# Performance work log

Measured on AMD Instinct MI355X. Metric: run time of the kernel, lower is better.

## Reference

```python
import jax, jax.numpy as jnp
import numpy as np

B, L, D = 4, 1024, 1024
H = 16
HD = D // H
SCALE = HD ** -0.5
LOCAL_WINDOW = 32
HALF = LOCAL_WINDOW // 2
TEMP = 1.0
PATTERN_TEMP = 1.0
THRESHOLD = 0.1
SPARSITY_RATIO = 0.3
# k for learned sparse topk (eval mode, static given L)
EFF = min(SPARSITY_RATIO, 1.0 - 10.0 / L)
K_TOP = max(1, min(L, int(L * (1.0 - EFF))))


def setup_inputs() -> dict:
    key = jax.random.key(0)
    ks = jax.random.split(key, 16)
    def xavier(k, shape, gain=1.0):
        fan_in, fan_out = shape[1], shape[0]
        a = gain * np.sqrt(6.0 / (fan_in + fan_out))
        return jax.random.uniform(k, shape, jnp.float32, -a, a)
    return {
        'x': jax.random.normal(ks[0], (B, L, D), jnp.float32),
        'w_qkv': xavier(ks[1], (3 * D, D), gain=1.0 / np.sqrt(2.0)),
        'w_proj': xavier(ks[2], (D, D)),
        'b_proj': jnp.zeros((D,), jnp.float32),
        'ps_w1': xavier(ks[3], (D, D), gain=0.5),
        'ps_b1': jnp.zeros((D,), jnp.float32),
        'ln_g': jnp.ones((D,), jnp.float32),
        'ln_b': jnp.zeros((D,), jnp.float32),
        'ps_w2': xavier(ks[4], (D // 2, D), gain=0.5),
        'ps_b2': jnp.zeros((D // 2,), jnp.float32),
        'ps_w3': xavier(ks[5], (3, D // 2), gain=0.5),
        'ps_b3': jnp.zeros((3,), jnp.float32),
        'pattern_bias': jnp.array([0.05, 0.0, -0.05], jnp.float32),
        'sparse_w': jax.random.normal(ks[6], (H, 1, 1), jnp.float32) * 0.1 + 1.0,
        'sparse_b': jnp.zeros((H, 1, 1), jnp.float32),
    }


def _forward(x, w_qkv, w_proj, b_proj, ps_w1, ps_b1, ln_g, ln_b,
             ps_w2, ps_b2, ps_w3, ps_b3, pattern_bias, sparse_w, sparse_b):
    qkv = (x @ w_qkv.T).reshape(B, L, 3, H, HD)
    qkv = jnp.transpose(qkv, (2, 0, 3, 1, 4))  # [3,B,H,L,HD]
    q, k, v = qkv[0], qkv[1], qkv[2]
    scores = jnp.einsum('bhid,bhjd->bhij', q, k) * SCALE  # [B,H,L,L]

    # pattern selector on pooled features
    pooled = (jnp.mean(x, axis=1) + jnp.max(x, axis=1)) / 2.0  # [B,D]
    h = pooled @ ps_w1.T + ps_b1
    mu = jnp.mean(h, axis=-1, keepdims=True)
    var = jnp.mean((h - mu) ** 2, axis=-1, keepdims=True)
    h = (h - mu) / jnp.sqrt(var + 1e-5) * ln_g + ln_b
    h = jax.nn.gelu(h, approximate=False)
    h = jax.nn.gelu(h @ ps_w2.T + ps_b2, approximate=False)
    logits = h @ ps_w3.T + ps_b3 + pattern_bias  # [B,3]
    pw = jax.nn.softmax(logits / PATTERN_TEMP, axis=-1)  # [B,3]

    # learned sparse mask via per-head affine + topk scatter
    s2 = scores * jnp.abs(sparse_w)[None] + sparse_b[None]  # [B,H,L,L]
    _, topk_idx = jax.lax.top_k(s2, K_TOP)  # [B,H,L,K]
    bi = jnp.arange(B)[:, None, None, None]
    hi = jnp.arange(H)[None, :, None, None]
    li = jnp.arange(L)[None, None, :, None]
    sparse_mask = jnp.zeros_like(scores).at[bi, hi, li, topk_idx].set(1.0)

    # local sliding-window mask |i-j| <= HALF
    i = jnp.arange(L)
    local = (jnp.abs(i[:, None] - i[None, :]) <= HALF).astype(jnp.float32)  # [L,L]

    combined = (pw[:, 0, None, None, None] * local[None, None]
                + pw[:, 1, None, None, None]
                + pw[:, 2, None, None, None] * sparse_mask)
    binary = combined > THRESHOLD
    scores = jnp.where(binary, scores, -jnp.inf)

    # fallback: rows fully masked attend only to themselves (score 0)
    all_masked = ~jnp.any(binary, axis=-1)  # [B,H,L]
    eye = jnp.eye(L, dtype=bool)
    scores = jnp.where(all_masked[..., None] & eye[None, None], 0.0, scores)

    attn = jax.nn.softmax(scores / TEMP, axis=-1)
    out = jnp.einsum('bhij,bhjd->bhid', attn, v)  # [B,H,L,HD]
    out = jnp.transpose(out, (0, 2, 1, 3)).reshape(B, L, D)
    return out @ w_proj.T + b_proj


def reference(x, w_qkv, w_proj, b_proj, ps_w1, ps_b1, ln_g, ln_b,
              ps_w2, ps_b2, ps_w3, ps_b3, pattern_bias, sparse_w, sparse_b):
    return _forward(x, w_qkv, w_proj, b_proj, ps_w1, ps_b1, ln_g, ln_b,
                    ps_w2, ps_b2, ps_w3, ps_b3, pattern_bias, sparse_w, sparse_b)
```

## Files before the change

### kernel.cpp

```cpp
#include <hip/hip_runtime.h>
#include <math.h>

#define KTOP_ 716
#define SCALE_ 0.125f
#define QSCALE_ 0.1803368801111731f
#define LN2_ 0.6931471805599453f

typedef float f4v __attribute__((ext_vector_type(4)));
typedef short s8v __attribute__((ext_vector_type(8)));
typedef __bf16 bf8v __attribute__((ext_vector_type(8)));

static __device__ inline unsigned short f2bf(float f) {
  unsigned u = __float_as_uint(f);
  u += 0x7fffu + ((u >> 16) & 1u);
  return (unsigned short)(u >> 16);
}
static __device__ inline unsigned short f2bfn(float f) {
  union { __bf16 b; unsigned short u; } cv;
  cv.b = (__bf16)f;
  return cv.u;
}
static __device__ inline float bf2f(unsigned short h) {
  return __uint_as_float((unsigned)h << 16);
}
static __device__ inline f4v mfma16(s8v a, s8v b, f4v c) {
  union { s8v s; bf8v b; } ua, ub;
  ua.s = a; ub.s = b;
  return __builtin_amdgcn_mfma_f32_16x16x32_bf16(ua.b, ub.b, c, 0, 0, 0);
}
static __device__ inline void gload16(const unsigned short* g, unsigned short* lbase) {
  __builtin_amdgcn_global_load_lds(
      (const __attribute__((address_space(1))) unsigned int*)g,
      (__attribute__((address_space(3))) unsigned int*)lbase, 16, 0, 0);
}

__global__ __launch_bounds__(256) void pool1(const float* __restrict__ x,
                                             float* __restrict__ psum,
                                             float* __restrict__ pmax,
                                             unsigned short* __restrict__ xs) {
  int bid = blockIdx.x;
  int b = bid >> 6, sl = bid & 63;
  int t = threadIdx.x;
  float s[4] = {0.f, 0.f, 0.f, 0.f};
  float m[4] = {-INFINITY, -INFINITY, -INFINITY, -INFINITY};
  const float* xb = x + ((size_t)b << 20) + (size_t)sl * 16 * 1024;
  unsigned short* xo = xs + ((size_t)(b * 1024 + sl * 16)) * 1024;
  for (int l = 0; l < 16; ++l) {
    #pragma unroll
    for (int dg = 0; dg < 4; ++dg) {
      float v = xb[l * 1024 + dg * 256 + t];
      s[dg] += v;
      m[dg] = fmaxf(m[dg], v);
      xo[(size_t)l * 1024 + dg * 256 + t] = f2bfn(v);
    }
  }
  #pragma unroll
  for (int dg = 0; dg < 4; ++dg) {
    psum[(size_t)bid * 1024 + dg * 256 + t] = s[dg];
    pmax[(size_t)bid * 1024 + dg * 256 + t] = m[dg];
  }
}

__global__ __launch_bounds__(256) void ps_gemv1(const float* __restrict__ psum,
                                                const float* __restrict__ pmax,
                                                const float* __restrict__ w1,
                                                const float* __restrict__ b1,
                                                float* __restrict__ h1) {
  __shared__ float pool_s[1024];
  int bid = blockIdx.x;
  int b = bid >> 4, og = bid & 15;
  int t = threadIdx.x;
  #pragma unroll
  for (int i = 0; i < 4; ++i) {
    int d = t + 256 * i;
    float s = 0.f, m = -INFINITY;
    #pragma unroll 8
    for (int sl = 0; sl < 64; ++sl) {
      s += psum[((size_t)b * 64 + sl) * 1024 + d];
      m = fmaxf(m, pmax[((size_t)b * 64 + sl) * 1024 + d]);
    }
    pool_s[d] = (s * (1.0f / 1024.0f) + m) * 0.5f;
  }
  __syncthreads();
  int ol = t >> 2, ks = t & 3;
  int o = og * 64 + ol;
  const float4* wr = (const float4*)(w1 + (size_t)o * 1024 + ks * 256);
  const float4* pp = (const float4*)(&pool_s[ks * 256]);
  float acc = 0.f;
  #pragma unroll 8
  for (int j = 0; j < 64; ++j) {
    float4 a = wr[j], p = pp[j];
    acc += a.x * p.x + a.y * p.y + a.z * p.z + a.w * p.w;
  }
  acc += __shfl_xor(acc, 1, 64);
  acc += __shfl_xor(acc, 2, 64);
  if (ks == 0) h1[b * 1024 + o] = acc + b1[o];
}

__global__ __launch_bounds__(256) void ps_gemv2(const float* __restrict__ h1,
                                                const float* __restrict__ lng,
                                                const float* __restrict__ lnb,
                                                const float* __restrict__ w2,
                                                const float* __restrict__ b2,
                                                float* __restrict__ h2) {
  __shared__ float hs[1024];
  __shared__ float red[256];
  int bid = blockIdx.x;
  int b = bid >> 3, og = bid & 7;
  int t = threadIdx.x;
  const float* hb = h1 + b * 1024;
  float v0[4];
  float ls = 0.f;
  #pragma unroll
  for (int i = 0; i < 4; ++i) { v0[i] = hb[t + 256 * i]; ls += v0[i]; }
  red[t] = ls; __syncthreads();
  for (int s = 128; s > 0; s >>= 1) { if (t < s) red[t] += red[t + s]; __syncthreads(); }
  float mean = red[0] * (1.0f / 1024.0f);
  __syncthreads();
  float lq = 0.f;
  #pragma unroll
  for (int i = 0; i < 4; ++i) { float dv = v0[i] - mean; lq += dv * dv; }
  red[t] = lq; __syncthreads();
  for (int s = 128; s > 0; s >>= 1) { if (t < s) red[t] += red[t + s]; __syncthreads(); }
  float rstd = 1.0f / sqrtf(red[0] * (1.0f / 1024.0f) + 1e-5f);
  #pragma unroll
  for (int i = 0; i < 4; ++i) {
    float v = (v0[i] - mean) * rstd * lng[t + 256 * i] + lnb[t + 256 * i];
    hs[t + 256 * i] = 0.5f * v * (1.0f + erff(v * 0.70710678118654752f));
  }
  __syncthreads();
  int ol = t >> 2, ks = t & 3;
  int o = og * 64 + ol;
  const float4* wr = (const float4*)(w2 + (size_t)o * 1024 + ks * 256);
  const float4* pp = (const float4*)(&hs[ks * 256]);
  float acc = 0.f;
  #pragma unroll 8
  for (int j = 0; j < 64; ++j) {
    float4 a = wr[j], p = pp[j];
    acc += a.x * p.x + a.y * p.y + a.z * p.z + a.w * p.w;
  }
  acc += __shfl_xor(acc, 1, 64);
  acc += __shfl_xor(acc, 2, 64);
  if (ks == 0) {
    float v = acc + b2[o];
    h2[b * 512 + o] = 0.5f * v * (1.0f + erff(v * 0.70710678118654752f));
  }
}

__global__ __launch_bounds__(256) void ps_logits(const float* __restrict__ h2,
                                                 const float* __restrict__ w3,
                                                 const float* __restrict__ b3,
                                                 const float* __restrict__ pb,
                                                 int* __restrict__ meta) {
  __shared__ float red[256];
  int b = blockIdx.x, t = threadIdx.x;
  float lgv[3];
  for (int c = 0; c < 3; ++c) {
    float p = 0.f;
    for (int i = t; i < 512; i += 256) p += h2[b * 512 + i] * w3[c * 512 + i];
    red[t] = p; __syncthreads();
    for (int s = 128; s > 0; s >>= 1) { if (t < s) red[t] += red[t + s]; __syncthreads(); }
    lgv[c] = red[0] + b3[c] + pb[c];
    __syncthreads();
  }
  if (t == 0) {
    float mx = fmaxf(lgv[0], fmaxf(lgv[1], lgv[2]));
    float e0 = __expf(lgv[0] - mx), e1 = __expf(lgv[1] - mx), e2 = __expf(lgv[2] - mx);
    float inv = 1.0f / (e0 + e1 + e2);
    float p0 = e0 * inv, p1 = e1 * inv, p2 = e2 * inv;
    float c00 = p1;
    float c10 = p0 + p1;
    float c01 = p1 + p2;
    float c11 = (p0 + p1) + p2;
    int t00 = c00 > 0.1f, t10 = c10 > 0.1f, t01 = c01 > 0.1f, t11 = c11 > 0.1f;
    meta[b * 8 + 0] = t00;
    meta[b * 8 + 1] = t10;
    meta[b * 8 + 2] = t01;
    meta[b * 8 + 3] = t11;
    meta[b * 8 + 4] = (t00 != t01) || (t10 != t11);
  }
}

__global__ __launch_bounds__(256) void prep_w(const float* __restrict__ w_qkv,
                                              const float* __restrict__ w_proj,
                                              unsigned short* __restrict__ wqs,
                                              unsigned short* __restrict__ wps) {
  int i = blockIdx.x * 256 + threadIdx.x;
  const float* src;
  unsigned short* dst;
  int idx;
  if (i < 786432) { src = w_qkv; dst = wqs; idx = i; }
  else            { src = w_proj; dst = wps; idx = i - 786432; }
  float4 v = ((const float4*)src)[idx];
  ushort4 o;
  o.x = f2bfn(v.x); o.y = f2bfn(v.y); o.z = f2bfn(v.z); o.w = f2bfn(v.w);
  *(ushort4*)(dst + (size_t)idx * 4) = o;
}

template <int MODE, int TM>
__global__ __launch_bounds__(256) void gemm_sp(
    const unsigned short* __restrict__ A, const unsigned short* __restrict__ B,
    const float* __restrict__ bias,
    unsigned short* __restrict__ qxo, unsigned short* __restrict__ kxo,
    unsigned short* __restrict__ vxo,
    float* __restrict__ out, int Nb) {
  constexpr int MFR = TM / 32;
  __shared__ unsigned short Asm[2][TM * 64];
  __shared__ unsigned short Bsm[2][128 * 64];

  int bid = blockIdx.x;
  int bm, bn;
  if (MODE == 0) {
    int xcd = bid & 7, idx = bid >> 3;
    int rb = (xcd >> 1) * 8, cb = (xcd & 1) * 12;
    int r, c;
    if (idx < 64) { r = idx & 7; c = idx >> 3; }
    else          { int j = idx - 64; r = j & 7; c = 8 + (j >> 3); }
    bm = rb + r; bn = cb + c;
  } else {
    int cpx = gridDim.x >> 3;
    int g = (bid & 7) * cpx + (bid >> 3);
    bm = g / Nb; bn = g % Nb;
  }
  size_t row0 = (size_t)bm * TM, col0 = (size_t)bn * 128;

  int tid = threadIdx.x, lane = tid & 63, wv = tid >> 6;
  int wm = (wv >> 1) * (MFR * 16), wn = (wv & 1) << 6;
  int rowg = lane >> 4, colc = lane & 15;

  f4v acc[MFR][4];
  #pragma unroll
  for (int mf = 0; mf < MFR; ++mf)
    #pragma unroll
    for (int nf = 0; nf < 4; ++nf) acc[mf][nf] = (f4v){0.f, 0.f, 0.f, 0.f};

  const unsigned short* Abase = A + row0 * 1024;
  const unsigned short* Bbase = B + col0 * 1024;

  auto STAGE = [&](int kb, int buf) {
    #pragma unroll
    for (int p = 0; p < TM / 32; ++p) {
      int idx = p * 256 + tid;
      int row = idx >> 3;
      int sc = (idx & 7) ^ (row & 7);
      gload16(Abase + (size_t)row * 1024 + kb + sc * 8,
              &Asm[buf][(size_t)(p * 256 + wv * 64) * 8]);
    }
    #pragma unroll
    for (int p = 0; p < 4; ++p) {
      int idx = p * 256 + tid;
      int row = idx >> 3;
      int sc = (idx & 7) ^ (row & 7);
      gload16(Bbase + (size_t)row * 1024 + kb + sc * 8,
              &Bsm[buf][(size_t)(p * 256 + wv * 64) * 8]);
    }
  };

  STAGE(0, 0);
  __syncthreads();
  int cur = 0;

  for (int kb = 0; kb < 1024; kb += 64) {
    if (kb + 64 < 1024) STAGE(kb + 64, cur ^ 1);
    #pragma unroll
    for (int ks = 0; ks < 2; ++ks) {
      s8v af[MFR], bf_[4];
      #pragma unroll
      for (int mf = 0; mf < MFR; ++mf) {
        int row = wm + mf * 16 + colc;
        int kby = (ks * 64 + rowg * 16) ^ ((row & 7) << 4);
        af[mf] = *(const s8v*)((const char*)&Asm[cur][0] + row * 128 + kby);
      }
      #pragma unroll
      for (int nf = 0; nf < 4; ++nf) {
        int row = wn + nf * 16 + colc;
        int kby = (ks * 64 + rowg * 16) ^ ((row & 7) << 4);
        bf_[nf] = *(const s8v*)((const char*)&Bsm[cur][0] + row * 128 + kby);
      }
      #pragma unroll
      for (int mf = 0; mf < MFR; ++mf)
        #pragma unroll
        for (int nf = 0; nf < 4; ++nf)
          acc[mf][nf] = mfma16(af[mf], bf_[nf], acc[mf][nf]);
    }
    __syncthreads();
    cur ^= 1;
  }

  if (MODE == 0) {
    int c = (int)(col0 >> 10);
    #pragma unroll
    for (int mf = 0; mf < MFR; ++mf) {
      int m0 = (int)row0 + wm + mf * 16 + rowg * 4;
      int bb = m0 >> 10, l0 = m0 & 1023;
      #pragma unroll
      for (int nf = 0; nf < 4; ++nf) {
        int n = (int)col0 + wn + nf * 16 + colc;
        int hh = (n >> 6) & 15, hd = n & 63;
        int bhl = bb * 16 + hh;
        if (c == 2) {
          ushort4 h4;
          h4.x = f2bfn(acc[mf][nf][0]);
          h4.y = f2bfn(acc[mf][nf][1]);
          h4.z = f2bfn(acc[mf][nf][2]);
          h4.w = f2bfn(acc[mf][nf][3]);
          *(ushort4*)(vxo + ((size_t)bhl * 64 + hd) * 1024 + l0) = h4;
        } else {
          unsigned short* dst = ((c == 0) ? qxo : kxo) +
                                ((size_t)bhl * 1024 + l0) * 64 + hd;
          float sc_ = (c == 0) ? QSCALE_ : 1.0f;
          #pragma unroll
          for (int r = 0; r < 4; ++r)
            dst[(size_t)r * 64] = f2bfn(acc[mf][nf][r] * sc_);
        }
      }
    }
  } else {
    #pragma unroll
    for (int mf = 0; mf < MFR; ++mf) {
      #pragma unroll
      for (int r = 0; r < 4; ++r) {
        int m = (int)row0 + wm + mf * 16 + rowg * 4 + r;
        #pragma unroll
        for (int nf = 0; nf < 4; ++nf) {
          int n = (int)col0 + wn + nf * 16 + colc;
          out[(size_t)m * 1024 + n] = acc[mf][nf][r] + bias[n];
        }
      }
    }
  }
}

__global__ __launch_bounds__(512) void attn_flash(
    const unsigned short* __restrict__ qx, const unsigned short* __restrict__ kx,
    const unsigned short* __restrict__ vx, const int* __restrict__ meta,
    unsigned short* __restrict__ ao) {
  int n = blockIdx.x;
  int bh = ((n & 7) << 3) | (n >> 6);
  int qt2 = (n >> 3) & 7;
  int b = bh >> 4, h = bh & 15;
  const int* mb = meta + b * 8;
  if (mb[4]) return;
  int t00 = mb[0], t10 = mb[1];

  int tid = threadIdx.x, lane = tid & 63, wv = tid >> 6;
  int g = lane >> 4, colc = lane & 15;
  int bq0 = qt2 * 128;
  int q0 = bq0 + wv * 16;

  if (!t10) {
    #pragma unroll
    for (int it = 0; it < 4; ++it) {
      int idx = tid + it * 512;
      int r = idx >> 4, dc = (idx & 15) * 4;
      ushort4 o;
      unsigned short* op = (unsigned short*)&o;
      #pragma unroll
      for (int j = 0; j < 4; ++j)
        op[j] = vx[((size_t)bh * 64 + dc + j) * 1024 + bq0 + r];
      *(ushort4*)(ao + ((size_t)b * 1024 + bq0 + r) * 1024 + h * 64 + dc) = o;
    }
    return;
  }
  bool local_only = !t00;

  __shared__ __align__(16) unsigned short KsmA[64 * 64];
  __shared__ __align__(16) unsigned short KsmB[64 * 64];
  __shared__ __align__(16) unsigned short VsmA[64 * 64];
  __shared__ __align__(16) unsigned short VsmB[64 * 64];
  __shared__ __align__(16) unsigned short px[8][16][64];

  const unsigned short* qb = qx + ((size_t)bh * 1024 + q0 + colc) * 64 + g * 8;
  s8v Q0 = *(const s8v*)(qb);
  s8v Q1 = *(const s8v*)(qb + 32);

  f4v O[4];
  #pragma unroll
  for (int df = 0; df < 4; ++df) O[df] = (f4v){0.f, 0.f, 0.f, 0.f};
  float m = -1e30f, lsum = 0.f;

  const unsigned short* kxb = kx + ((size_t)bh << 10) * 64;
  const unsigned short* vxb = vx + ((size_t)bh << 16);

  int jb_lo = 0, jb_hi = 15;
  if (local_only) {
    int lo = (bq0 - 16) >> 6, hi = (bq0 + 143) >> 6;
    jb_lo = lo < 0 ? 0 : lo;
    jb_hi = hi > 15 ? 15 : hi;
  }

  int srow = tid >> 3;
  int ssc = (tid & 7) ^ (srow & 7);
  auto STAGE = [&](int jb2, unsigned short* Kd, unsigned short* Vd) {
    int jc = jb2 << 6;
    unsigned short* lbase_k = Kd + (size_t)(wv * 64) * 8;
    unsigned short* lbase_v = Vd + (size_t)(wv * 64) * 8;
    gload16(kxb + (size_t)(jc + srow) * 64 + ssc * 8, lbase_k);
    gload16(vxb + (size_t)srow * 1024 + jc + ssc * 8, lbase_v);
  };

  int swk = (colc & 7) << 4;
  int sx = (colc & 7) << 1;

  auto COMPUTE = [&](int jc0, const char* Kb, const char* Vb) {
    if (local_only && (jc0 + 63 < q0 - 16 || jc0 > q0 + 31)) return;
    f4v s[4];
    __builtin_amdgcn_s_setprio(1);
    #pragma unroll
    for (int jf = 0; jf < 4; ++jf) {
      const char* kp = Kb + (jf * 16 + colc) * 128;
      s8v K0 = *(const s8v*)(kp + ((g * 16) ^ swk));
      s8v K1 = *(const s8v*)(kp + ((64 + g * 16) ^ swk));
      f4v acc = (f4v){0.f, 0.f, 0.f, 0.f};
      acc = mfma16(K0, Q0, acc);
      acc = mfma16(K1, Q1, acc);
      s[jf] = acc;
    }
    __builtin_amdgcn_s_setprio(0);

    if (local_only) {
      int i = q0 + colc;
      #pragma unroll
      for (int jf = 0; jf < 4; ++jf)
        #pragma unroll
        for (int r = 0; r < 4; ++r) {
          int j = jc0 + jf * 16 + 4 * g + r;
          int dj = i - j;
          if (dj > 16 || dj < -16) s[jf][r] = -1e30f;
        }
    }

    float cm = fmaxf(
        fmaxf(fmaxf(fmaxf(s[0][0], s[0][1]), fmaxf(s[0][2], s[0][3])),
              fmaxf(fmaxf(s[1][0], s[1][1]), fmaxf(s[1][2], s[1][3]))),
        fmaxf(fmaxf(fmaxf(s[2][0], s[2][1]), fmaxf(s[2][2], s[2][3])),
              fmaxf(fmaxf(s[3][0], s[3][1]), fmaxf(s[3][2], s[3][3]))));
    cm = fmaxf(cm, __shfl_xor(cm, 16, 64));
    cm = fmaxf(cm, __shfl_xor(cm, 32, 64));

    if (__any(cm > m + 8.0f)) {
      float mn = fmaxf(m, cm);
      float fac = __builtin_amdgcn_exp2f(m - mn);
      m = mn;
      lsum *= fac;
      float fo[4];
      #pragma unroll
      for (int r = 0; r < 4; ++r)
        fo[r] = __shfl(fac, (lane & 48) + g * 4 + r, 64);
      #pragma unroll
      for (int df = 0; df < 4; ++df)
        #pragma unroll
        for (int r = 0; r < 4; ++r) O[df][r] *= fo[r];
    }

    float psum = 0.f;
    #pragma unroll
    for (int jf = 0; jf < 4; ++jf) {
      float p0 = __builtin_amdgcn_exp2f(s[jf][0] - m);
      float p1 = __builtin_amdgcn_exp2f(s[jf][1] - m);
      float p2 = __builtin_amdgcn_exp2f(s[jf][2] - m);
      float p3 = __builtin_amdgcn_exp2f(s[jf][3] - m);
      psum += (p0 + p1) + (p2 + p3);
      ushort4 pk;
      pk.x = f2bfn(p0); pk.y = f2bfn(p1); pk.z = f2bfn(p2); pk.w = f2bfn(p3);
      *(ushort4*)&px[wv][colc][4 * ((jf * 4 + g) ^ sx)] = pk;
    }
    psum += __shfl_xor(psum, 16, 64);
    psum += __shfl_xor(psum, 32, 64);
    lsum += psum;

    s8v Pf[2];
    #pragma unroll
    for (int ks = 0; ks < 2; ++ks)
      Pf[ks] = *(const s8v*)&px[wv][colc][4 * ((ks * 8 + 2 * g) ^ sx)];
    __builtin_amdgcn_s_setprio(1);
    #pragma unroll
    for (int df = 0; df < 4; ++df) {
      const char* vp = Vb + (df * 16 + colc) * 128;
      #pragma unroll
      for (int ks = 0; ks < 2; ++ks) {
        s8v Vf = *(const s8v*)(vp + ((ks * 64 + g * 16) ^ swk));
        O[df] = mfma16(Pf[ks], Vf, O[df]);
      }
    }
    __builtin_amdgcn_s_setprio(0);
  };

  STAGE(jb_lo, KsmA, VsmA);
  __syncthreads();
  int jb = jb_lo;
  while (true) {
    if (jb + 1 <= jb_hi) STAGE(jb + 1, KsmB, VsmB);
    COMPUTE(jb << 6, (const char*)KsmA, (const char*)VsmA);
    __syncthreads();
    ++jb;
    if (jb > jb_hi) break;
    if (jb + 1 <= jb_hi) STAGE(jb + 1, KsmA, VsmA);
    COMPUTE(jb << 6, (const char*)KsmB, (const char*)VsmB);
    __syncthreads();
    ++jb;
    if (jb > jb_hi) break;
  }

  float linv[4];
  #pragma unroll
  for (int r = 0; r < 4; ++r)
    linv[r] = 1.0f / __shfl(lsum, (lane & 48) + g * 4 + r, 64);
  #pragma unroll
  for (int df = 0; df < 4; ++df) {
    #pragma unroll
    for (int r = 0; r < 4; ++r) {
      int i = q0 + g * 4 + r;
      ao[((size_t)b * 1024 + i) * 1024 + h * 64 + df * 16 + colc] =
          f2bfn(O[df][r] * linv[r]);
    }
  }
}

__global__ __launch_bounds__(256) void attn_sparse(
    const unsigned short* __restrict__ qx, const unsigned short* __restrict__ kx,
    const unsigned short* __restrict__ vx, const int* __restrict__ meta,
    unsigned short* __restrict__ ao) {
  __shared__ float S[32][1028];
  __shared__ float qs[32][68];
  __shared__ float kc[64][68];
  __shared__ float rowsum_s[32];

  int tid = threadIdx.x;
  int lane = tid & 63;
  int wv = tid >> 6;
  int id = blockIdx.x;
  int rt = id & 31;
  int h = (id >> 5) & 15;
  int b = id >> 9;
  int bh = b * 16 + h;
  int row0 = rt * 32;

  const int* mb = meta + b * 8;
  int t00 = mb[0], t10 = mb[1], t01 = mb[2], t11 = mb[3], needs = mb[4];
  if (!needs) return;

  #pragma unroll
  for (int i = 0; i < 8; ++i) {
    int idx = tid + 256 * i;
    int r = idx >> 6, d = idx & 63;
    qs[r][d] = bf2f(qx[((size_t)bh * 1024 + row0 + r) * 64 + d]);
  }

  int lr = lane >> 4, lc = lane & 15;
  int r_a = wv * 8 + lr * 2;
  int r_b = r_a + 1;

  for (int cb = 0; cb < 16; ++cb) {
    __syncthreads();
    #pragma unroll
    for (int i = 0; i < 2; ++i) {
      int idx = tid + 256 * i;
      int cc = idx >> 3, d0 = (idx & 7) * 8;
      union { s8v v; unsigned short u[8]; } kv8;
      kv8.v = *(const s8v*)(kx + ((size_t)bh * 1024 + cb * 64 + cc) * 64 + d0);
      #pragma unroll
      for (int j = 0; j < 8; ++j) kc[cc][d0 + j] = bf2f(kv8.u[j]);
    }
    __syncthreads();

    float acc0[4] = {0.f, 0.f, 0.f, 0.f};
    float acc1[4] = {0.f, 0.f, 0.f, 0.f};
    for (int dq = 0; dq < 64; dq += 4) {
      float4 qa = *(const float4*)&qs[r_a][dq];
      float4 qb = *(const float4*)&qs[r_b][dq];
      #pragma unroll
      for (int cj = 0; cj < 4; ++cj) {
        float4 kv = *(const float4*)&kc[lc + 16 * cj][dq];
        acc0[cj] += qa.x * kv.x + qa.y * kv.y + qa.z * kv.z + qa.w * kv.w;
        acc1[cj] += qb.x * kv.x + qb.y * kv.y + qb.z * kv.z + qb.w * kv.w;
      }
    }
    #pragma unroll
    for (int cj = 0; cj < 4; ++cj) {
      S[r_a][cb * 64 + lc + 16 * cj] = acc0[cj] * LN2_;
      S[r_b][cb * 64 + lc + 16 * cj] = acc1[cj] * LN2_;
    }
  }

  for (int rr = 0; rr < 8; ++rr) {
    int r = wv * 8 + rr;
    int grow = row0 + r;
    float sv[16];
    unsigned kv[16];
    #pragma unroll
    for (int i2 = 0; i2 < 16; ++i2) {
      float s = S[r][lane + 64 * i2];
      sv[i2] = s;
      unsigned u = __float_as_uint(s);
      kv[i2] = (u & 0x80000000u) ? ~u : (u | 0x80000000u);
    }
    unsigned T = 0u;
    for (int bit = 31; bit >= 0; --bit) {
      unsigned cand = T | (1u << bit);
      int cnt = 0;
      #pragma unroll
      for (int i2 = 0; i2 < 16; ++i2) cnt += (kv[i2] >= cand) ? 1 : 0;
      for (int off = 32; off; off >>= 1) cnt += __shfl_xor(cnt, off, 64);
      if (cnt >= KTOP_) T = cand;
    }
    float mx = -INFINITY;
    int kept = 0;
    unsigned kmask = 0;
    #pragma unroll
    for (int i2 = 0; i2 < 16; ++i2) {
      int j = lane + 64 * i2;
      int sp = (kv[i2] >= T) ? 1 : 0;
      int dj = grow - j;
      int lo = (dj <= 16 && dj >= -16) ? 1 : 0;
      int keep = sp ? (lo ? t11 : t01) : (lo ? t10 : t00);
      kept += keep;
      if (keep) { kmask |= (1u << i2); mx = fmaxf(mx, sv[i2]); }
    }
    for (int off = 32; off; off >>= 1) {
      mx = fmaxf(mx, __shfl_xor(mx, off, 64));
      kept += __shfl_xor(kept, off, 64);
    }
    if (kept == 0) {
      #pragma unroll
      for (int i2 = 0; i2 < 16; ++i2) {
        int j = lane + 64 * i2;
        S[r][j] = (j == grow) ? 1.0f : 0.0f;
      }
      if (lane == 0) rowsum_s[r] = 1.0f;
    } else {
      float sum = 0.f;
      #pragma unroll
      for (int i2 = 0; i2 < 16; ++i2) {
        float p = ((kmask >> i2) & 1u) ? __expf(sv[i2] - mx) : 0.0f;
        sum += p;
        S[r][lane + 64 * i2] = p;
      }
      for (int off = 32; off; off >>= 1) sum += __shfl_xor(sum, off, 64);
      if (lane == 0) rowsum_s[r] = sum;
    }
  }

  int ld = lane & 15;
  int d0 = ld * 4;
  float4 oa0 = make_float4(0.f, 0.f, 0.f, 0.f);
  float4 oa1 = make_float4(0.f, 0.f, 0.f, 0.f);
  for (int vb = 0; vb < 16; ++vb) {
    __syncthreads();
    #pragma unroll
    for (int i = 0; i < 2; ++i) {
      int idx = tid + 256 * i;
      int d = idx >> 3, c0 = (idx & 7) * 8;
      union { s8v v; unsigned short u[8]; } vv8;
      vv8.v = *(const s8v*)(vx + ((size_t)bh * 64 + d) * 1024 + vb * 64 + c0);
      #pragma unroll
      for (int j = 0; j < 8; ++j) kc[c0 + j][d] = bf2f(vv8.u[j]);
    }
    __syncthreads();
    for (int cq = 0; cq < 64; cq += 4) {
      float4 pa = *(const float4*)&S[r_a][vb * 64 + cq];
      float4 pb = *(const float4*)&S[r_b][vb * 64 + cq];
      float par[4] = {pa.x, pa.y, pa.z, pa.w};
      float pbr[4] = {pb.x, pb.y, pb.z, pb.w};
      #pragma unroll
      for (int tt = 0; tt < 4; ++tt) {
        float4 vv = *(const float4*)&kc[cq + tt][d0];
        oa0.x += par[tt] * vv.x; oa0.y += par[tt] * vv.y;
        oa0.z += par[tt] * vv.z; oa0.w += par[tt] * vv.w;
        oa1.x += pbr[tt] * vv.x; oa1.y += pbr[tt] * vv.y;
        oa1.z += pbr[tt] * vv.z; oa1.w += pbr[tt] * vv.w;
      }
    }
  }
  float inv0 = 1.0f / rowsum_s[r_a];
  float inv1 = 1.0f / rowsum_s[r_b];
  ushort4 o0, o1;
  unsigned short* o0p = (unsigned short*)&o0;
  unsigned short* o1p = (unsigned short*)&o1;
  float v0[4] = {oa0.x * inv0, oa0.y * inv0, oa0.z * inv0, oa0.w * inv0};
  float v1[4] = {oa1.x * inv1, oa1.y * inv1, oa1.z * inv1, oa1.w * inv1};
  #pragma unroll
  for (int j = 0; j < 4; ++j) {
    o0p[j] = f2bf(v0[j]);
    o1p[j] = f2bf(v1[j]);
  }
  *(ushort4*)(ao + ((size_t)b * 1024 + row0 + r_a) * 1024 + h * 64 + d0) = o0;
  *(ushort4*)(ao + ((size_t)b * 1024 + row0 + r_b) * 1024 + h * 64 + d0) = o1;
}

__global__ __launch_bounds__(256) void pool_kernel(const float* __restrict__ x,
                                                   float* __restrict__ pooled) {
  int g = blockIdx.x * 256 + threadIdx.x;
  int b = g >> 10, d = g & 1023;
  const float* xp = x + ((size_t)b << 20) + d;
  float s = 0.f, m = -INFINITY;
  #pragma unroll 4
  for (int l = 0; l < 1024; ++l) {
    float v = xp[(size_t)l << 10];
    s += v;
    m = fmaxf(m, v);
  }
  pooled[g] = (s * (1.0f / 1024.0f) + m) * 0.5f;
}

__global__ __launch_bounds__(256) void qkv_gemm(const float* __restrict__ X,
                                                const float* __restrict__ W,
                                                float* __restrict__ qw,
                                                float* __restrict__ kw,
                                                float* __restrict__ vw) {
  __shared__ float As[8][128];
  __shared__ float Bs[8][128];
  int tid = threadIdx.x;
  int row0 = blockIdx.y * 128, col0 = blockIdx.x * 128;
  int lr = tid >> 1;
  int lk = (tid & 1) * 4;
  int ty = tid >> 4, tx = tid & 15;
  float acc[8][8] = {};

  for (int kb = 0; kb < 1024; kb += 8) {
    float4 a4 = *(const float4*)(X + (size_t)(row0 + lr) * 1024 + kb + lk);
    float4 b4 = *(const float4*)(W + (size_t)(col0 + lr) * 1024 + kb + lk);
    __syncthreads();
    As[lk + 0][lr] = a4.x; As[lk + 1][lr] = a4.y; As[lk + 2][lr] = a4.z; As[lk + 3][lr] = a4.w;
    Bs[lk + 0][lr] = b4.x; Bs[lk + 1][lr] = b4.y; Bs[lk + 2][lr] = b4.z; Bs[lk + 3][lr] = b4.w;
    __syncthreads();
    #pragma unroll
    for (int kk = 0; kk < 8; ++kk) {
      float av[8], bv[8];
      #pragma unroll
      for (int i = 0; i < 8; ++i) av[i] = As[kk][ty * 8 + i];
      #pragma unroll
      for (int j = 0; j < 8; ++j) bv[j] = Bs[kk][tx * 8 + j];
      #pragma unroll
      for (int i = 0; i < 8; ++i)
        #pragma unroll
        for (int j = 0; j < 8; ++j) acc[i][j] += av[i] * bv[j];
    }
  }
  #pragma unroll
  for (int i = 0; i < 8; ++i) {
    int m = row0 + ty * 8 + i;
    int bb = m >> 10, l = m & 1023;
    #pragma unroll
    for (int j = 0; j < 8; j += 4) {
      int n = col0 + tx * 8 + j;
      int c = n >> 10;
      int hh = (n >> 6) & 15;
      int hd = n & 63;
      float* base = (c == 0) ? qw : (c == 1) ? kw : vw;
      float* dst = base + ((size_t)(bb * 16 + hh) * 1024 + l) * 64 + hd;
      *(float4*)dst = make_float4(acc[i][j], acc[i][j + 1], acc[i][j + 2], acc[i][j + 3]);
    }
  }
}

__global__ __launch_bounds__(256) void proj_gemm(const float* __restrict__ A,
                                                 const float* __restrict__ W,
                                                 const float* __restrict__ bias,
                                                 float* __restrict__ out) {
  __shared__ float As[8][128];
  __shared__ float Bs[8][128];
  int tid = threadIdx.x;
  int row0 = blockIdx.y * 128, col0 = blockIdx.x * 128;
  int lr = tid >> 1;
  int lk = (tid & 1) * 4;
  int ty = tid >> 4, tx = tid & 15;
  float acc[8][8] = {};

  for (int kb = 0; kb < 1024; kb += 8) {
    float4 a4 = *(const float4*)(A + (size_t)(row0 + lr) * 1024 + kb + lk);
    float4 b4 = *(const float4*)(W + (size_t)(col0 + lr) * 1024 + kb + lk);
    __syncthreads();
    As[lk + 0][lr] = a4.x; As[lk + 1][lr] = a4.y; As[lk + 2][lr] = a4.z; As[lk + 3][lr] = a4.w;
    Bs[lk + 0][lr] = b4.x; Bs[lk + 1][lr] = b4.y; Bs[lk + 2][lr] = b4.z; Bs[lk + 3][lr] = b4.w;
    __syncthreads();
    #pragma unroll
    for (int kk = 0; kk < 8; ++kk) {
      float av[8], bv[8];
      #pragma unroll
      for (int i = 0; i < 8; ++i) av[i] = As[kk][ty * 8 + i];
      #pragma unroll
      for (int j = 0; j < 8; ++j) bv[j] = Bs[kk][tx * 8 + j];
      #pragma unroll
      for (int i = 0; i < 8; ++i)
        #pragma unroll
        for (int j = 0; j < 8; ++j) acc[i][j] += av[i] * bv[j];
    }
  }
  #pragma unroll
  for (int i = 0; i < 8; ++i) {
    int m = row0 + ty * 8 + i;
    #pragma unroll
    for (int j = 0; j < 8; j += 4) {
      int n = col0 + tx * 8 + j;
      *(float4*)(out + (size_t)m * 1024 + n) =
          make_float4(acc[i][j] + bias[n], acc[i][j + 1] + bias[n + 1],
                      acc[i][j + 2] + bias[n + 2], acc[i][j + 3] + bias[n + 3]);
    }
  }
}

__global__ __launch_bounds__(256) void pattern_kernel(
    const float* __restrict__ pooled,
    const float* __restrict__ w1, const float* __restrict__ b1,
    const float* __restrict__ lng, const float* __restrict__ lnb,
    const float* __restrict__ w2, const float* __restrict__ b2,
    const float* __restrict__ w3, const float* __restrict__ b3,
    const float* __restrict__ pb, int* __restrict__ meta) {
  __shared__ float pool_s[1024];
  __shared__ float h1[1024];
  __shared__ float h2[512];
  __shared__ float red[256];
  int b = blockIdx.x, t = threadIdx.x;

  for (int i = t; i < 1024; i += 256) pool_s[i] = pooled[b * 1024 + i];
  __syncthreads();
  for (int o = t; o < 1024; o += 256) {
    float acc = b1[o];
    const float* wr = w1 + (size_t)o * 1024;
    for (int k = 0; k < 1024; ++k) acc += pool_s[k] * wr[k];
    h1[o] = acc;
  }
  __syncthreads();
  float ls = 0.f;
  for (int i = t; i < 1024; i += 256) ls += h1[i];
  red[t] = ls; __syncthreads();
  for (int s = 128; s > 0; s >>= 1) { if (t < s) red[t] += red[t + s]; __syncthreads(); }
  float mean = red[0] * (1.0f / 1024.0f);
  __syncthreads();
  float lq = 0.f;
  for (int i = t; i < 1024; i += 256) { float dv = h1[i] - mean; lq += dv * dv; }
  red[t] = lq; __syncthreads();
  for (int s = 128; s > 0; s >>= 1) { if (t < s) red[t] += red[t + s]; __syncthreads(); }
  float var = red[0] * (1.0f / 1024.0f);
  float rstd = 1.0f / sqrtf(var + 1e-5f);
  __syncthreads();
  for (int i = t; i < 1024; i += 256) {
    float v = (h1[i] - mean) * rstd * lng[i] + lnb[i];
    h1[i] = 0.5f * v * (1.0f + erff(v * 0.70710678118654752f));
  }
  __syncthreads();
  for (int o = t; o < 512; o += 256) {
    float acc = b2[o];
    const float* wr = w2 + (size_t)o * 1024;
    for (int k = 0; k < 1024; ++k) acc += h1[k] * wr[k];
    h2[o] = 0.5f * acc * (1.0f + erff(acc * 0.70710678118654752f));
  }
  __syncthreads();
  float lgv[3];
  for (int c = 0; c < 3; ++c) {
    float p = 0.f;
    for (int i = t; i < 512; i += 256) p += h2[i] * w3[c * 512 + i];
    __syncthreads();
    red[t] = p; __syncthreads();
    for (int s = 128; s > 0; s >>= 1) { if (t < s) red[t] += red[t + s]; __syncthreads(); }
    lgv[c] = red[0] + b3[c] + pb[c];
  }
  if (t == 0) {
    float mx = fmaxf(lgv[0], fmaxf(lgv[1], lgv[2]));
    float e0 = __expf(lgv[0] - mx), e1 = __expf(lgv[1] - mx), e2 = __expf(lgv[2] - mx);
    float inv = 1.0f / (e0 + e1 + e2);
    float p0 = e0 * inv, p1 = e1 * inv, p2 = e2 * inv;
    float c00 = p1;
    float c10 = p0 + p1;
    float c01 = p1 + p2;
    float c11 = (p0 + p1) + p2;
    int t00 = c00 > 0.1f, t10 = c10 > 0.1f, t01 = c01 > 0.1f, t11 = c11 > 0.1f;
    meta[b * 8 + 0] = t00;
    meta[b * 8 + 1] = t10;
    meta[b * 8 + 2] = t01;
    meta[b * 8 + 3] = t11;
    meta[b * 8 + 4] = (t00 != t01) || (t10 != t11);
  }
}

__global__ __launch_bounds__(256) void attn_kernel_f32(const float* __restrict__ qw,
                                                       const float* __restrict__ kw,
                                                       const float* __restrict__ vw,
                                                       const int* __restrict__ meta,
                                                       float* __restrict__ ao) {
  __shared__ float S[32][1028];
  __shared__ float qs[32][68];
  __shared__ float kc[64][68];
  __shared__ float rowsum_s[32];

  int tid = threadIdx.x;
  int lane = tid & 63;
  int wv = tid >> 6;
  int id = blockIdx.x;
  int rt = id & 31;
  int h = (id >> 5) & 15;
  int b = id >> 9;
  int bh = b * 16 + h;
  int row0 = rt * 32;

  const int* mb = meta + b * 8;
  int t00 = mb[0], t10 = mb[1], t01 = mb[2], t11 = mb[3], needs = mb[4];

  {
    const float4* qp = (const float4*)(qw + ((size_t)bh * 1024 + row0 + wv * 8) * 64);
    #pragma unroll
    for (int i = 0; i < 2; ++i) {
      int f = lane + 64 * i;
      float4 v = qp[f];
      int r = wv * 8 + (f >> 4);
      int d = (f & 15) << 2;
      qs[r][d] = v.x; qs[r][d + 1] = v.y; qs[r][d + 2] = v.z; qs[r][d + 3] = v.w;
    }
  }

  int lr = lane >> 4, lc = lane & 15;
  int r_a = wv * 8 + lr * 2;
  int r_b = r_a + 1;

  for (int cb = 0; cb < 16; ++cb) {
    __syncthreads();
    const float4* kp = (const float4*)(kw + ((size_t)bh * 1024 + cb * 64) * 64);
    #pragma unroll
    for (int i = 0; i < 4; ++i) {
      int f = tid + 256 * i;
      float4 v = kp[f];
      int c = f >> 4, d = (f & 15) << 2;
      kc[c][d] = v.x; kc[c][d + 1] = v.y; kc[c][d + 2] = v.z; kc[c][d + 3] = v.w;
    }
    __syncthreads();

    float acc0[4] = {0.f, 0.f, 0.f, 0.f};
    float acc1[4] = {0.f, 0.f, 0.f, 0.f};
    for (int dq = 0; dq < 64; dq += 4) {
      float4 qa = *(const float4*)&qs[r_a][dq];
      float4 qb = *(const float4*)&qs[r_b][dq];
      #pragma unroll
      for (int cj = 0; cj < 4; ++cj) {
        float4 kv = *(const float4*)&kc[lc + 16 * cj][dq];
        acc0[cj] += qa.x * kv.x + qa.y * kv.y + qa.z * kv.z + qa.w * kv.w;
        acc1[cj] += qb.x * kv.x + qb.y * kv.y + qb.z * kv.z + qb.w * kv.w;
      }
    }
    #pragma unroll
    for (int cj = 0; cj < 4; ++cj) {
      S[r_a][cb * 64 + lc + 16 * cj] = acc0[cj] * SCALE_;
      S[r_b][cb * 64 + lc + 16 * cj] = acc1[cj] * SCALE_;
    }
  }

  for (int rr = 0; rr < 8; ++rr) {
    int r = wv * 8 + rr;
    int grow = row0 + r;
    float sv[16];
    unsigned kv[16];
    #pragma unroll
    for (int i2 = 0; i2 < 16; ++i2) {
      float s = S[r][lane + 64 * i2];
      sv[i2] = s;
      unsigned u = __float_as_uint(s);
      kv[i2] = (u & 0x80000000u) ? ~u : (u | 0x80000000u);
    }
    unsigned T = 0u;
    if (needs) {
      for (int bit = 31; bit >= 0; --bit) {
        unsigned cand = T | (1u << bit);
        int cnt = 0;
        #pragma unroll
        for (int i2 = 0; i2 < 16; ++i2) cnt += (kv[i2] >= cand) ? 1 : 0;
        for (int off = 32; off; off >>= 1) cnt += __shfl_xor(cnt, off, 64);
        if (cnt >= KTOP_) T = cand;
      }
    }
    float mx = -INFINITY;
    int kept = 0;
    unsigned kmask = 0;
    #pragma unroll
    for (int i2 = 0; i2 < 16; ++i2) {
      int j = lane + 64 * i2;
      int sp = (kv[i2] >= T) ? 1 : 0;
      int dj = grow - j;
      int lo = (dj <= 16 && dj >= -16) ? 1 : 0;
      int keep = sp ? (lo ? t11 : t01) : (lo ? t10 : t00);
      kept += keep;
      if (keep) { kmask |= (1u << i2); mx = fmaxf(mx, sv[i2]); }
    }
    for (int off = 32; off; off >>= 1) {
      mx = fmaxf(mx, __shfl_xor(mx, off, 64));
      kept += __shfl_xor(kept, off, 64);
    }
    if (kept == 0) {
      #pragma unroll
      for (int i2 = 0; i2 < 16; ++i2) {
        int j = lane + 64 * i2;
        S[r][j] = (j == grow) ? 1.0f : 0.0f;
      }
      if (lane == 0) rowsum_s[r] = 1.0f;
    } else {
      float sum = 0.f;
      #pragma unroll
      for (int i2 = 0; i2 < 16; ++i2) {
        float p = ((kmask >> i2) & 1u) ? __expf(sv[i2] - mx) : 0.0f;
        sum += p;
        S[r][lane + 64 * i2] = p;
      }
      for (int off = 32; off; off >>= 1) sum += __shfl_xor(sum, off, 64);
      if (lane == 0) rowsum_s[r] = sum;
    }
  }

  int ld = lane & 15;
  int d0 = ld * 4;
  float4 oa0 = make_float4(0.f, 0.f, 0.f, 0.f);
  float4 oa1 = make_float4(0.f, 0.f, 0.f, 0.f);
  for (int vb = 0; vb < 16; ++vb) {
    __syncthreads();
    const float4* vp = (const float4*)(vw + ((size_t)bh * 1024 + vb * 64) * 64);
    #pragma unroll
    for (int i = 0; i < 4; ++i) {
      int f = tid + 256 * i;
      float4 v = vp[f];
      int c = f >> 4, d = (f & 15) << 2;
      kc[c][d] = v.x; kc[c][d + 1] = v.y; kc[c][d + 2] = v.z; kc[c][d + 3] = v.w;
    }
    __syncthreads();
    for (int cq = 0; cq < 64; cq += 4) {
      float4 pa = *(const float4*)&S[r_a][vb * 64 + cq];
      float4 pb = *(const float4*)&S[r_b][vb * 64 + cq];
      float par[4] = {pa.x, pa.y, pa.z, pa.w};
      float pbr[4] = {pb.x, pb.y, pb.z, pb.w};
      #pragma unroll
      for (int tt = 0; tt < 4; ++tt) {
        float4 vv = *(const float4*)&kc[cq + tt][d0];
        oa0.x += par[tt] * vv.x; oa0.y += par[tt] * vv.y;
        oa0.z += par[tt] * vv.z; oa0.w += par[tt] * vv.w;
        oa1.x += pbr[tt] * vv.x; oa1.y += pbr[tt] * vv.y;
        oa1.z += pbr[tt] * vv.z; oa1.w += pbr[tt] * vv.w;
      }
    }
  }
  float inv0 = 1.0f / rowsum_s[r_a];
  float inv1 = 1.0f / rowsum_s[r_b];
  float* p0 = ao + ((size_t)b * 1024 + row0 + r_a) * 1024 + h * 64 + d0;
  float* p1 = ao + ((size_t)b * 1024 + row0 + r_b) * 1024 + h * 64 + d0;
  *(float4*)p0 = make_float4(oa0.x * inv0, oa0.y * inv0, oa0.z * inv0, oa0.w * inv0);
  *(float4*)p1 = make_float4(oa1.x * inv1, oa1.y * inv1, oa1.z * inv1, oa1.w * inv1);
}

extern "C" void kernel_launch(void* const* d_in, const int* in_sizes, int n_in,
                              void* d_out, int out_size, void* d_ws, size_t ws_size,
                              hipStream_t stream) {
  const float* x      = (const float*)d_in[0];
  const float* w_qkv  = (const float*)d_in[1];
  const float* w_proj = (const float*)d_in[2];
  const float* b_proj = (const float*)d_in[3];
  const float* ps_w1  = (const float*)d_in[4];
  const float* ps_b1  = (const float*)d_in[5];
  const float* ln_g   = (const float*)d_in[6];
  const float* ln_b   = (const float*)d_in[7];
  const float* ps_w2  = (const float*)d_in[8];
  const float* ps_b2  = (const float*)d_in[9];
  const float* ps_w3  = (const float*)d_in[10];
  const float* ps_b3  = (const float*)d_in[11];
  const float* pbias  = (const float*)d_in[12];

  float* ws = (float*)d_ws;
  float* pooled = ws;
  int*   meta   = (int*)(ws + 4096);
  float* h1buf  = ws + 8192;
  float* h2buf  = ws + 12288;
  float* ppsum  = ws + 16384;
  float* ppmax  = ws + 278528;
  float* qw = ws + 1048576;
  float* kw = qw + 4194304;
  float* vw = kw + 4194304;
  float* ao = vw + 4194304;
  unsigned short* u16b = (unsigned short*)(ao + 4194304);
  unsigned short* xs   = u16b;
  unsigned short* wqs  = xs + 4194304;
  unsigned short* wps  = wqs + 3145728;
  unsigned short* aos  = wps + 1048576;
  unsigned short* qx   = aos + 4194304;
  unsigned short* kx   = qx + 4194304;
  unsigned short* vx   = kx + 4194304;
  float* out = (float*)d_out;

  const size_t NEED_FULL = (size_t)(1048576 + 4 * 4194304) * 4 +
                           (size_t)(4194304 + 3145728 + 1048576 + 4194304 +
                                    3 * 4194304) * 2;

  if (ws_size >= NEED_FULL) {
    pool1<<<256, 256, 0, stream>>>(x, ppsum, ppmax, xs);
    ps_gemv1<<<64, 256, 0, stream>>>(ppsum, ppmax, ps_w1, ps_b1, h1buf);
    ps_gemv2<<<32, 256, 0, stream>>>(h1buf, ln_g, ln_b, ps_w2, ps_b2, h2buf);
    ps_logits<<<4, 256, 0, stream>>>(h2buf, ps_w3, ps_b3, pbias, meta);

    prep_w<<<4096, 256, 0, stream>>>(w_qkv, w_proj, wqs, wps);
    gemm_sp<0, 128><<<768, 256, 0, stream>>>(xs, wqs, nullptr, qx, kx, vx,
                                             nullptr, 24);

    attn_flash<<<512, 512, 0, stream>>>(qx, kx, vx, meta, aos);
    attn_sparse<<<2048, 256, 0, stream>>>(qx, kx, vx, meta, aos);

    gemm_sp<1, 64><<<512, 256, 0, stream>>>(aos, wps, b_proj,
                                            nullptr, nullptr, nullptr, out, 8);
  } else {
    pool_kernel<<<16, 256, 0, stream>>>(x, pooled);
    pattern_kernel<<<4, 256, 0, stream>>>(pooled, ps_w1, ps_b1, ln_g, ln_b,
                                          ps_w2, ps_b2, ps_w3, ps_b3, pbias, meta);
    qkv_gemm<<<dim3(24, 32), 256, 0, stream>>>(x, w_qkv, qw, kw, vw);
    attn_kernel_f32<<<2048, 256, 0, stream>>>(qw, kw, vw, meta, ao);
    proj_gemm<<<dim3(8, 32), 256, 0, stream>>>(ao, w_proj, b_proj, out);
  }
}
```

Before: 140.1 us.

## Use explicit vmcnt waits and raw barriers to overlap prefetch with MFMA

Restructures the GEMM main loop into a ping-pong over two named LDS buffers. Each step issues the next tile's global->LDS loads, then waits with a partial s_waitcnt vmcnt, so only the current tile's loads must finish before compute. The same partial-wait pattern replaces __syncthreads in the local attention loop, and MFMA blocks are wrapped in s_setprio. The goal is to keep the next tile's loads in flight during compute rather than draining all memory ops at each barrier. The hardcoded vmcnt counts depend on the exact number of loads per stage, so a miscount would cause data races.

```diff
diff --git a/kernel.cpp b/kernel.cpp
--- a/kernel.cpp
+++ b/kernel.cpp
@@ -5,6 +5,13 @@
 #define SCALE_ 0.125f
 #define QSCALE_ 0.1803368801111731f
 #define LN2_ 0.6931471805599453f
+
+#define WAIT_VMCNT(n) asm volatile("s_waitcnt vmcnt(" #n ")" ::: "memory")
+static __device__ inline void SBAR() {
+  __builtin_amdgcn_sched_barrier(0);
+  __builtin_amdgcn_s_barrier();
+  __builtin_amdgcn_sched_barrier(0);
+}
 
 typedef float f4v __attribute__((ext_vector_type(4)));
 typedef short s8v __attribute__((ext_vector_type(8)));
@@ -205,8 +212,10 @@
     unsigned short* __restrict__ vxo,
     float* __restrict__ out, int Nb) {
   constexpr int MFR = TM / 32;
-  __shared__ unsigned short Asm[2][TM * 64];
-  __shared__ unsigned short Bsm[2][128 * 64];
+  __shared__ unsigned short AsmA[TM * 64];
+  __shared__ unsigned short AsmB[TM * 64];
+  __shared__ unsigned short BsmA[128 * 64];
+  __shared__ unsigned short BsmB[128 * 64];
 
   int bid = blockIdx.x;
   int bm, bn;
@@ -237,14 +246,14 @@
   const unsigned short* Abase = A + row0 * 1024;
   const unsigned short* Bbase = B + col0 * 1024;
 
-  auto STAGE = [&](int kb, int buf) {
+  auto STAGE = [&](int kb, unsigned short* Ad, unsigned short* Bd) {
     #pragma unroll
     for (int p = 0; p < TM / 32; ++p) {
       int idx = p * 256 + tid;
       int row = idx >> 3;
       int sc = (idx & 7) ^ (row & 7);
       gload16(Abase + (size_t)row * 1024 + kb + sc * 8,
-              &Asm[buf][(size_t)(p * 256 + wv * 64) * 8]);
+              Ad + (size_t)(p * 256 + wv * 64) * 8);
     }
     #pragma unroll
     for (int p = 0; p < 4; ++p) {
@@ -252,16 +261,11 @@
       int row = idx >> 3;
       int sc = (idx & 7) ^ (row & 7);
       gload16(Bbase + (size_t)row * 1024 + kb + sc * 8,
-              &Bsm[buf][(size_t)(p * 256 + wv * 64) * 8]);
+              Bd + (size_t)(p * 256 + wv * 64) * 8);
     }
   };
 
-  STAGE(0, 0);
-  __syncthreads();
-  int cur = 0;
-
-  for (int kb = 0; kb < 1024; kb += 64) {
-    if (kb + 64 < 1024) STAGE(kb + 64, cur ^ 1);
+  auto COMPUTE = [&](const unsigned short* Ab, const unsigned short* Bb) {
     #pragma unroll
     for (int ks = 0; ks < 2; ++ks) {
       s8v af[MFR], bf_[4];
@@ -269,22 +273,40 @@
       for (int mf = 0; mf < MFR; ++mf) {
         int row = wm + mf * 16 + colc;
         int kby = (ks * 64 + rowg * 16) ^ ((row & 7) << 4);
-        af[mf] = *(const s8v*)((const char*)&Asm[cur][0] + row * 128 + kby);
+        af[mf] = *(const s8v*)((const char*)Ab + row * 128 + kby);
       }
       #pragma unroll
       for (int nf = 0; nf < 4; ++nf) {
         int row = wn + nf * 16 + colc;
         int kby = (ks * 64 + rowg * 16) ^ ((row & 7) << 4);
-        bf_[nf] = *(const s8v*)((const char*)&Bsm[cur][0] + row * 128 + kby);
-      }
+        bf_[nf] = *(const s8v*)((const char*)Bb + row * 128 + kby);
+      }
+      __builtin_amdgcn_s_setprio(1);
       #pragma unroll
       for (int mf = 0; mf < MFR; ++mf)
         #pragma unroll
         for (int nf = 0; nf < 4; ++nf)
           acc[mf][nf] = mfma16(af[mf], bf_[nf], acc[mf][nf]);
-    }
-    __syncthreads();
-    cur ^= 1;
+      __builtin_amdgcn_s_setprio(0);
+    }
+  };
+
+  STAGE(0, AsmA, BsmA);
+  for (int kb = 0; kb < 1024; kb += 128) {
+    STAGE(kb + 64, AsmB, BsmB);
+    if constexpr (TM == 128) WAIT_VMCNT(8); else WAIT_VMCNT(6);
+    SBAR();
+    COMPUTE(AsmA, BsmA);
+    SBAR();
+    if (kb + 128 < 1024) {
+      STAGE(kb + 128, AsmA, BsmA);
+      if constexpr (TM == 128) WAIT_VMCNT(8); else WAIT_VMCNT(6);
+    } else {
+      WAIT_VMCNT(0);
+    }
+    SBAR();
+    COMPUTE(AsmB, BsmB);
+    SBAR();
   }
 
   if (MODE == 0) {
@@ -487,19 +509,20 @@
   };
 
   STAGE(jb_lo, KsmA, VsmA);
-  __syncthreads();
   int jb = jb_lo;
   while (true) {
-    if (jb + 1 <= jb_hi) STAGE(jb + 1, KsmB, VsmB);
+    if (jb + 1 <= jb_hi) { STAGE(jb + 1, KsmB, VsmB); WAIT_VMCNT(2); }
+    else                 { WAIT_VMCNT(0); }
+    SBAR();
     COMPUTE(jb << 6, (const char*)KsmA, (const char*)VsmA);
-    __syncthreads();
-    ++jb;
-    if (jb > jb_hi) break;
-    if (jb + 1 <= jb_hi) STAGE(jb + 1, KsmA, VsmA);
+    SBAR();
+    if (++jb > jb_hi) break;
+    if (jb + 1 <= jb_hi) { STAGE(jb + 1, KsmA, VsmA); WAIT_VMCNT(2); }
+    else                 { WAIT_VMCNT(0); }
+    SBAR();
     COMPUTE(jb << 6, (const char*)KsmB, (const char*)VsmB);
-    __syncthreads();
-    ++jb;
-    if (jb > jb_hi) break;
+    SBAR();
+    if (++jb > jb_hi) break;
   }
 
   float linv[4];
```

Result: faster. 135.9 us (-3.0%).
